# Kernel tuning notes

Hardware: AMD Instinct MI355X
Metric: run time of the kernel (lower is better)

Reference implementation:

```python
import jax, jax.numpy as jnp
import numpy as np

K = 60           # output_size (num tags)
START_TAG = 58
STOP_TAG = 59
NEG = -10000.0


def _conv1d(x, w, b, pad):
    # x: (B, Cin, T), w: (Cout, Cin, k) -> (B, Cout, T)
    y = jax.lax.conv_general_dilated(x, w, (1,), [(pad, pad)],
                                     dimension_numbers=('NCH', 'OIH', 'NCH'))
    return y + b[None, :, None]


def _cnn_feats(sentence, w1, b1, w2, b2, w3, b3, w4, b4, w5, b5, fc_w, fc_b):
    # sentence: (T, B, 3) -> (B, 3, T)
    x = jnp.transpose(sentence, (1, 2, 0))
    in2 = jax.nn.relu(_conv1d(x, w1, b1, 1))
    in3 = jax.nn.relu(_conv1d(in2, w2, b2, 1))
    in4 = jax.nn.relu(_conv1d(in3 + in2, w3, b3, 1))
    in5 = jax.nn.relu(_conv1d(in4 + in3, w4, b4, 1))
    c5 = jax.nn.relu(_conv1d(in5 + in4, w5, b5, 2))
    h = jnp.transpose(c5, (2, 0, 1))                 # (T, B, H)
    return jnp.einsum('tbh,kh->tbk', h, fc_w) + fc_b  # (T, B, K)


def _viterbi(feats, trans):
    Bsz = feats.shape[1]
    fv0 = jnp.full((Bsz, K), NEG, dtype=feats.dtype).at[:, START_TAG].set(0.0)

    def step(fv, feat):
        # scores[b, next, prev] = fv[b, prev] + trans[next, prev]
        scores = fv[:, None, :] + trans[None, :, :]
        bptr = jnp.argmax(scores, axis=2)             # (B, K)
        fv_new = jnp.max(scores, axis=2) + feat       # (B, K)
        return fv_new, bptr

    fv, bptrs = jax.lax.scan(step, fv0, feats)        # bptrs: (T, B, K)
    terminal = fv + trans[STOP_TAG]                   # (B, K)
    path_score = jnp.max(terminal, axis=1)            # (B,)
    best_last = jnp.argmax(terminal, axis=1)          # (B,)

    def back(tag, bp):
        prev = jnp.take_along_axis(bp, tag[:, None], axis=1)[:, 0]
        return prev, tag

    _, best_path = jax.lax.scan(back, best_last, bptrs, reverse=True)  # (T, B)
    return path_score, best_path


def setup_inputs() -> dict:
    key = jax.random.key(0)
    ks = jax.random.split(key, 14)
    T, B, HID = 8192, 2, 512

    def u(k, shape, fan_in):
        bound = 1.0 / np.sqrt(fan_in).astype(np.float32)
        return jax.random.uniform(k, shape, minval=-bound, maxval=bound, dtype=jnp.float32)

    sentence = jax.random.normal(ks[0], (T, B, 3), dtype=jnp.float32)
    w1 = u(ks[1], (HID, 3, 3), 3 * 3);      b1 = u(ks[2], (HID,), 3 * 3)
    w2 = u(ks[3], (HID, HID, 3), HID * 3);  b2 = u(ks[4], (HID,), HID * 3)
    w3 = u(ks[5], (HID, HID, 3), HID * 3);  b3 = u(ks[6], (HID,), HID * 3)
    w4 = u(ks[7], (HID, HID, 3), HID * 3);  b4 = u(ks[8], (HID,), HID * 3)
    w5 = u(ks[9], (HID, HID, 5), HID * 5);  b5 = u(ks[10], (HID,), HID * 5)
    fc_w = u(ks[11], (K, HID), HID);        fc_b = u(ks[12], (K,), HID)

    trans = jax.random.normal(ks[13], (K, K), dtype=jnp.float32)
    m = np.zeros((K, K), dtype=bool)
    m[START_TAG, :] = True
    m[:, STOP_TAG] = True
    for i in range(2, K):
        for j in range(2, K):
            if j <= i or j >= i + 2:
                m[j, i] = True
    trans = jnp.where(jnp.asarray(m), jnp.float32(NEG), trans)

    return {'sentence': sentence,
            'w1': w1, 'b1': b1, 'w2': w2, 'b2': b2, 'w3': w3, 'b3': b3,
            'w4': w4, 'b4': b4, 'w5': w5, 'b5': b5,
            'fc_w': fc_w, 'fc_b': fc_b, 'trans': trans}


def reference(sentence, w1, b1, w2, b2, w3, b3, w4, b4, w5, b5, fc_w, fc_b, trans):
    feats = _cnn_feats(sentence, w1, b1, w2, b2, w3, b3, w4, b4, w5, b5, fc_w, fc_b)
    path_score, best_path = _viterbi(feats, trans)
    return path_score, best_path
```

## Files before the change

### kernel.cpp

```cpp
#include <hip/hip_runtime.h>

#define BATCH 2
#define HID 512
#define KTAGS 60
#define NEGV -10000.0f
#define NINF -3.0e38f

template<int CTRL>
__device__ __forceinline__ float dmax(float x) {
    int r = __builtin_amdgcn_update_dpp(__float_as_int(x), __float_as_int(x),
                                        CTRL, 0xf, 0xf, false);
    return fmaxf(x, __int_as_float(r));
}
template<int CTRL>
__device__ __forceinline__ float dmov(float x, float old) {
    int r = __builtin_amdgcn_update_dpp(__float_as_int(old), __float_as_int(x),
                                        CTRL, 0xf, 0xf, false);
    return __int_as_float(r);
}

__device__ __forceinline__ void heater(const int* done) {
    float a0 = 1.0f, a1 = 1.1f, a2 = 1.2f, a3 = 1.3f;
    float a4 = 1.4f, a5 = 1.5f, a6 = 1.6f, a7 = 1.7f;
    const float c = 1.0000001f, d = 1e-7f;
    for (int i = 0; i < 600000; ++i) {
        a0 = fmaf(a0, c, d); a1 = fmaf(a1, c, d); a2 = fmaf(a2, c, d); a3 = fmaf(a3, c, d);
        a4 = fmaf(a4, c, d); a5 = fmaf(a5, c, d); a6 = fmaf(a6, c, d); a7 = fmaf(a7, c, d);
        if ((i & 255) == 255) {
            if (__hip_atomic_load(done, __ATOMIC_RELAXED, __HIP_MEMORY_SCOPE_AGENT) >= BATCH)
                break;
        }
    }
    asm volatile("" :: "v"(a0), "v"(a1), "v"(a2), "v"(a3),
                       "v"(a4), "v"(a5), "v"(a6), "v"(a7));
}

__global__ __launch_bounds__(256) void conv1_kernel(
    const float* __restrict__ sent, const float* __restrict__ w1,
    const float* __restrict__ b1, float* __restrict__ y, int T, int B)
{
    const int t0 = blockIdx.x * 256;
    const int c0 = blockIdx.y * 8;
    const int b = blockIdx.z;
    __shared__ float S[3][258];
    const int tid = threadIdx.x;
    for (int i = tid; i < 3 * 258; i += 256) {
        int tt = i / 3, ci = i % 3;
        int t = t0 - 1 + tt;
        S[ci][tt] = (t >= 0 && t < T) ? sent[(size_t)t * (B * 3) + b * 3 + ci] : 0.f;
    }
    __syncthreads();
    const int t = t0 + tid;
    float x[3][3];
#pragma unroll
    for (int dk = 0; dk < 3; ++dk)
#pragma unroll
        for (int ci = 0; ci < 3; ++ci)
            x[dk][ci] = S[ci][tid + dk];
#pragma unroll
    for (int c = 0; c < 8; ++c) {
        int cc = c0 + c;
        float acc = b1[cc];
#pragma unroll
        for (int dk = 0; dk < 3; ++dk)
#pragma unroll
            for (int ci = 0; ci < 3; ++ci)
                acc += x[dk][ci] * w1[cc * 9 + ci * 3 + dk];
        y[((size_t)b * HID + cc) * T + t] = fmaxf(acc, 0.f);
    }
}

__global__ __launch_bounds__(256) void wtrans_kernel(
    const float* __restrict__ w, float* __restrict__ wt, int K)
{
    int idx = blockIdx.x * 256 + threadIdx.x;
    int total = HID * HID * K;
    if (idx >= total) return;
    int co = idx / (HID * K);
    int rem = idx % (HID * K);
    int ci = rem / K, dk = rem % K;
    wt[((size_t)ci * K + dk) * HID + co] = w[idx];
}

template<int KTAP, bool RES>
__global__ __launch_bounds__(256) void conv_kernel(
    const float* __restrict__ x1, const float* __restrict__ x2,
    const float* __restrict__ wt, const float* __restrict__ bias,
    float* __restrict__ y, int T)
{
    const int PAD = KTAP / 2;
    const int t0 = blockIdx.x * 64;
    const int co0 = blockIdx.y * 128;
    const int b = blockIdx.z;
    __shared__ float Xs[16][72];
    __shared__ float Ws[16][KTAP][128];
    const int tid = threadIdx.x;
    const int tx = tid & 15;
    const int ty = tid >> 4;
    float acc[8][4] = {};
    const size_t plane = (size_t)HID * T;
    const float* xa = x1 + (size_t)b * plane;
    const float* xb = RES ? (x2 + (size_t)b * plane) : nullptr;

    float xr[5];
    float4 wr[2 * KTAP];
    int xci[5], xtt[5];
#pragma unroll
    for (int k = 0; k < 5; ++k) {
        int i = tid + k * 256;
        xci[k] = i / 68;
        xtt[k] = i % 68;
    }

    auto load_stage = [&](int c0) {
#pragma unroll
        for (int k = 0; k < 5; ++k) {
            float v = 0.f;
            if (tid + k * 256 < 16 * 68) {
                int t = t0 + xtt[k] - 2;
                if (t >= 0 && t < T) {
                    size_t off = (size_t)(c0 + xci[k]) * T + t;
                    v = xa[off];
                    if (RES) v += xb[off];
                }
            }
            xr[k] = v;
        }
#pragma unroll
        for (int k = 0; k < 2 * KTAP; ++k) {
            int i = tid + k * 256;
            int c4 = i & 31, r = i >> 5;
            int dk = r % KTAP, ci = r / KTAP;
            wr[k] = *(const float4*)&wt[(((size_t)(c0 + ci) * KTAP + dk) * HID) + co0 + c4 * 4];
        }
    };
    auto write_stage = [&]() {
#pragma unroll
        for (int k = 0; k < 5; ++k)
            if (tid + k * 256 < 16 * 68) Xs[xci[k]][xtt[k]] = xr[k];
#pragma unroll
        for (int k = 0; k < 2 * KTAP; ++k) {
            int i = tid + k * 256;
            int c4 = i & 31, r = i >> 5;
            int dk = r % KTAP, ci = r / KTAP;
            *(float4*)&Ws[ci][dk][c4 * 4] = wr[k];
        }
    };

    load_stage(0);
    for (int c0 = 0; c0 < HID; c0 += 16) {
        write_stage();
        __syncthreads();
        if (c0 + 16 < HID) load_stage(c0 + 16);
#pragma unroll 4
        for (int ci = 0; ci < 16; ++ci) {
            float f8[8];
            *(float4*)&f8[0] = *(const float4*)&Xs[ci][tx * 4];
            *(float4*)&f8[4] = *(const float4*)&Xs[ci][tx * 4 + 4];
#pragma unroll
            for (int dk = 0; dk < KTAP; ++dk) {
                float wv[8];
                *(float4*)&wv[0] = *(const float4*)&Ws[ci][dk][ty * 8];
                *(float4*)&wv[4] = *(const float4*)&Ws[ci][dk][ty * 8 + 4];
#pragma unroll
                for (int r = 0; r < 8; ++r)
#pragma unroll
                    for (int c = 0; c < 4; ++c)
                        acc[r][c] = fmaf(wv[r], f8[c + dk + (2 - PAD)], acc[r][c]);
            }
        }
        __syncthreads();
    }
#pragma unroll
    for (int r = 0; r < 8; ++r) {
        int co = co0 + ty * 8 + r;
        float bv = bias[co];
#pragma unroll
        for (int c = 0; c < 4; ++c) {
            int t = t0 + tx * 4 + c;
            float v = acc[r][c] + bv;
            y[(size_t)b * plane + (size_t)co * T + t] = fmaxf(v, 0.f);
        }
    }
}

__global__ __launch_bounds__(256) void fc_kernel(
    const float* __restrict__ x, const float* __restrict__ fw,
    const float* __restrict__ fb, float* __restrict__ feats, int* done, int T)
{
    int t0 = blockIdx.x * 64, b = blockIdx.y;
    if (t0 == 0 && b == 0 && threadIdx.x == 0)
        __hip_atomic_store(done, 0, __ATOMIC_RELAXED, __HIP_MEMORY_SCOPE_AGENT);
    __shared__ float Xs[64][65];
    __shared__ float Ws[64][60];
    int tid = threadIdx.x;
    int k = tid & 63, tq = tid >> 6;
    float acc[16] = {};
    const float* xb = x + (size_t)b * HID * T;
    for (int c0 = 0; c0 < HID; c0 += 64) {
        for (int i = tid; i < 64 * 64; i += 256) {
            int ci = i >> 6, tt = i & 63;
            Xs[ci][tt] = xb[(size_t)(c0 + ci) * T + t0 + tt];
        }
        for (int i = tid; i < 64 * 60; i += 256) {
            int kk = i % 60, ci = i / 60;
            Ws[ci][kk] = fw[(size_t)kk * HID + c0 + ci];
        }
        __syncthreads();
        if (k < KTAGS) {
#pragma unroll 8
            for (int ci = 0; ci < 64; ++ci) {
                float wv = Ws[ci][k];
#pragma unroll
                for (int i = 0; i < 16; ++i)
                    acc[i] = fmaf(wv, Xs[ci][tq * 16 + i], acc[i]);
            }
        }
        __syncthreads();
    }
    float bv = (k < KTAGS) ? fb[k] : 0.f;
#pragma unroll
    for (int i = 0; i < 16; ++i) {
        int t = t0 + tq * 16 + i;
        feats[((size_t)t * 2 + b) * 64 + k] = (k < KTAGS) ? acc[i] + bv : NINF;
    }
}

__global__ __launch_bounds__(256) void viterbi_fwd(
    const float* __restrict__ feats, const float* __restrict__ trans,
    float* __restrict__ fvbuf, int* done, int T)
{
    const int bid = blockIdx.x;
    const int tid = threadIdx.x;
    if (bid >= BATCH || tid >= 64) { heater(done); return; }
    __builtin_amdgcn_s_setprio(1);
    const int b = bid;
    const int l = tid;
    if (l >= 16) return;
    float tc0[4], tc1[4], trc[4], tr0[4], tr1[4], fv[4];
#pragma unroll
    for (int j = 0; j < 4; ++j) {
        int k = 4 * l + j;
        int kc = (k < KTAGS) ? k : (KTAGS - 1);
        bool real = (k < KTAGS);
        tc0[j] = trans[kc * KTAGS + 0];
        tc1[j] = trans[kc * KTAGS + 1];
        trc[j] = (kc >= 1) ? trans[kc * KTAGS + (kc - 1)] : NINF;
        tr0[j] = real ? trans[0 * KTAGS + kc] : NINF;
        tr1[j] = real ? trans[1 * KTAGS + kc] : NINF;
        fv[j]  = real ? ((k == 58) ? 0.f : NEGV) : NINF;
    }
    float fv0h = NEGV, fv1h = NEGV;
    {
        float4 st = {fv[0], fv[1], fv[2], fv[3]};
        *(float4*)&fvbuf[(size_t)b * 64 + 4 * l] = st;
    }
    const float* fp   = feats + b * 64 + 4 * l;
    const float* fp01 = feats + b * 64;
    float* fvp = fvbuf + 128 + b * 64 + 4 * l;

    auto step = [&](float4 f, float2 f01, int j, float* outp) {
        float p3 = dmov<0x111>(fv[3], fv[3]);
        float em0 = fmaxf(fv0h + tc0[0], fv1h + tc1[0]);
        float em1 = fmaxf(fv0h + tc0[1], fv1h + tc1[1]);
        float em2 = fmaxf(fv0h + tc0[2], fv1h + tc1[2]);
        float em3 = fmaxf(fv0h + tc0[3], fv1h + tc1[3]);
        float c1 = fv[0] + trc[1];
        float c2 = fv[1] + trc[2];
        float c3 = fv[2] + trc[3];
        float a0 = fmaxf(fmaxf(fv[0] + tr0[0], fv[1] + tr0[1]), fmaxf(fv[2] + tr0[2], fv[3] + tr0[3]));
        float a1 = fmaxf(fmaxf(fv[0] + tr1[0], fv[1] + tr1[1]), fmaxf(fv[2] + tr1[2], fv[3] + tr1[3]));
        float hi = fmaxf(fv[2], fv[3]);
        float m2 = ((l == 0) ? hi : fmaxf(fmaxf(fv[0], fv[1]), hi)) + NEGV;
        float c0 = p3 + trc[0];
        a0 = dmax<0xB1>(a0);  a1 = dmax<0xB1>(a1);  m2 = dmax<0xB1>(m2);
        a0 = dmax<0x4E>(a0);  a1 = dmax<0x4E>(a1);  m2 = dmax<0x4E>(m2);
        a0 = dmax<0x141>(a0); a1 = dmax<0x141>(a1); m2 = dmax<0x141>(m2);
        a0 = dmax<0x140>(a0); a1 = dmax<0x140>(a1); m2 = dmax<0x140>(m2);
        float nf0 = a0 + f01.x;
        float nf1 = a1 + f01.y;
        float g0 = fmaxf(em0, fmaxf(c0, m2)) + f.x;
        float g1 = fmaxf(em1, fmaxf(c1, m2)) + f.y;
        float g2 = fmaxf(em2, fmaxf(c2, m2)) + f.z;
        float g3 = fmaxf(em3, fmaxf(c3, m2)) + f.w;
        fv[0] = (l == 0) ? nf0 : g0;
        fv[1] = (l == 0) ? nf1 : g1;
        fv[2] = g2;
        fv[3] = g3;
        fv0h = nf0; fv1h = nf1;
        float4 st = {fv[0], fv[1], fv[2], fv[3]};
        *(float4*)&outp[j * 128] = st;
    };

    float4 fr[8];
    float2 fr2[8];
#pragma unroll
    for (int j = 0; j < 8; ++j) {
        fr[j]  = *(const float4*)&fp[j * 128];
        fr2[j] = *(const float2*)&fp01[j * 128];
    }
    fp += 8 * 128; fp01 += 8 * 128;

    for (int t = 0; t < T; t += 8) {
#pragma unroll
        for (int j = 0; j < 8; ++j) {
            step(fr[j], fr2[j], j, fvp);
            fr[j]  = *(const float4*)&fp[j * 128];
            fr2[j] = *(const float2*)&fp01[j * 128];
        }
        fp += 8 * 128; fp01 += 8 * 128;
        fvp += 8 * 128;
    }
    if (l == 0)
        __hip_atomic_fetch_add(done, 1, __ATOMIC_RELEASE, __HIP_MEMORY_SCOPE_AGENT);
}

__global__ __launch_bounds__(256) void bptr_kernel(
    const float* __restrict__ fvbuf, const float* __restrict__ trans,
    unsigned char* __restrict__ bp, int T)
{
    int b = blockIdx.y;
    int t0 = blockIdx.x * 16;
    __shared__ float trT[KTAGS][64];
    __shared__ float fvs[16][64];
    int tid = threadIdx.x;
    for (int i = tid; i < KTAGS * 64; i += 256) {
        int p = i >> 6, nx = i & 63;
        trT[p][nx] = (nx < KTAGS) ? trans[(size_t)nx * KTAGS + p] : NINF;
    }
    for (int i = tid; i < 16 * 64; i += 256) {
        int w = i >> 6, lx = i & 63;
        fvs[w][lx] = fvbuf[((size_t)(t0 + w) * 2 + b) * 64 + lx];
    }
    __syncthreads();
    int nx = tid & 63, w0 = tid >> 6;
    if (nx < KTAGS) {
#pragma unroll
        for (int j = 0; j < 4; ++j) {
            int w = w0 * 4 + j;
            float m = NINF; int am = 0;
            for (int p = 0; p < KTAGS; ++p) {
                float s = fvs[w][p] + trT[p][nx];
                if (s > m) { m = s; am = p; }
            }
            bp[((size_t)(t0 + w) * 2 + b) * 64 + nx] = (unsigned char)am;
        }
    }
}

__global__ __launch_bounds__(64) void vit_chunkmap(
    const unsigned char* __restrict__ bp, unsigned char* __restrict__ cmap)
{
    int c = blockIdx.x, b = blockIdx.y;
    __shared__ unsigned char bl[128][64];
    int tid = threadIdx.x;
    const unsigned int* src = (const unsigned int*)bp;
    for (int i = tid; i < 128 * 16; i += 64) {
        int row = i >> 4, q = i & 15;
        ((unsigned int*)&bl[row][0])[q] = src[((size_t)(c * 128 + row) * 2 + b) * 16 + q];
    }
    __syncthreads();
    if (tid < KTAGS) {
        int tag = tid;
#pragma unroll 1
        for (int i = 127; i >= 0; --i) tag = bl[i][tag];
        cmap[(c * 2 + b) * 64 + tid] = (unsigned char)tag;
    }
}

__global__ void vit_boundary(const unsigned char* __restrict__ cmap,
                             const float* __restrict__ fvbuf,
                             const float* __restrict__ trans,
                             int* __restrict__ xbound, float* __restrict__ out,
                             int nch, int T)
{
    int b = threadIdx.x;
    if (b < BATCH) {
        const float* fvT = fvbuf + ((size_t)T * 2 + b) * 64;
        float m = NINF; int am = 0;
        for (int p = 0; p < KTAGS; ++p) {
            float s = fvT[p] + trans[59 * KTAGS + p];
            if (s > m) { m = s; am = p; }
        }
        out[b] = m;
        int tag = am;
        for (int c = nch - 1; c >= 0; --c) {
            xbound[c * 2 + b] = tag;
            tag = cmap[(c * 2 + b) * 64 + tag];
        }
    }
}

__global__ __launch_bounds__(64) void vit_emit(
    const unsigned char* __restrict__ bp, const int* __restrict__ xbound,
    float* __restrict__ out)
{
    int c = blockIdx.x, b = blockIdx.y;
    __shared__ unsigned char bl[128][64];
    int tid = threadIdx.x;
    const unsigned int* src = (const unsigned int*)bp;
    for (int i = tid; i < 128 * 16; i += 64) {
        int row = i >> 4, q = i & 15;
        ((unsigned int*)&bl[row][0])[q] = src[((size_t)(c * 128 + row) * 2 + b) * 16 + q];
    }
    __syncthreads();
    if (tid == 0) {
        int tag = xbound[c * 2 + b];
        for (int i = 127; i >= 0; --i) {
            out[2 + (size_t)(c * 128 + i) * 2 + b] = (float)tag;
            tag = bl[i][tag];
        }
    }
}

extern "C" void kernel_launch(void* const* d_in, const int* in_sizes, int n_in,
                              void* d_out, int out_size, void* d_ws, size_t ws_size,
                              hipStream_t stream) {
    const float* sent = (const float*)d_in[0];
    const float* w1 = (const float*)d_in[1];  const float* b1 = (const float*)d_in[2];
    const float* w2 = (const float*)d_in[3];  const float* b2 = (const float*)d_in[4];
    const float* w3 = (const float*)d_in[5];  const float* b3 = (const float*)d_in[6];
    const float* w4 = (const float*)d_in[7];  const float* b4 = (const float*)d_in[8];
    const float* w5 = (const float*)d_in[9];  const float* b5 = (const float*)d_in[10];
    const float* fw = (const float*)d_in[11]; const float* fb = (const float*)d_in[12];
    const float* trans = (const float*)d_in[13];

    const int B = BATCH;
    const int T = in_sizes[0] / (B * 3);

    char* ws = (char*)d_ws;
    const size_t SZBUF = (size_t)2 * HID * 8192 * 4;
    float* bufA = (float*)(ws);
    float* bufB = (float*)(ws + SZBUF);
    float* bufC = (float*)(ws + 2 * SZBUF);
    float* wslot = (float*)(ws + 3 * SZBUF);
    float* feats = wslot;
    float* fvbuf = bufC;
    unsigned char* bp = (unsigned char*)ws;
    unsigned char* cmap = (unsigned char*)(ws + 2 * 1024 * 1024);
    int* xbound = (int*)(ws + 3 * 1024 * 1024);
    int* done = (int*)(ws + 3 * 1024 * 1024 + 65536);
    float* outp = (float*)d_out;

    conv1_kernel<<<dim3(T / 256, HID / 8, B), 256, 0, stream>>>(sent, w1, b1, bufA, T, B);

    wtrans_kernel<<<(HID * HID * 3 + 255) / 256, 256, 0, stream>>>(w2, wslot, 3);
    conv_kernel<3, false><<<dim3(T / 64, HID / 128, B), 256, 0, stream>>>(bufA, nullptr, wslot, b2, bufB, T);
    wtrans_kernel<<<(HID * HID * 3 + 255) / 256, 256, 0, stream>>>(w3, wslot, 3);
    conv_kernel<3, true ><<<dim3(T / 64, HID / 128, B), 256, 0, stream>>>(bufB, bufA, wslot, b3, bufC, T);
    wtrans_kernel<<<(HID * HID * 3 + 255) / 256, 256, 0, stream>>>(w4, wslot, 3);
    conv_kernel<3, true ><<<dim3(T / 64, HID / 128, B), 256, 0, stream>>>(bufC, bufB, wslot, b4, bufA, T);
    wtrans_kernel<<<(HID * HID * 5 + 255) / 256, 256, 0, stream>>>(w5, wslot, 5);
    conv_kernel<5, true ><<<dim3(T / 64, HID / 128, B), 256, 0, stream>>>(bufA, bufC, wslot, b5, bufB, T);

    fc_kernel<<<dim3(T / 64, B), 256, 0, stream>>>(bufB, fw, fb, feats, done, T);

    viterbi_fwd<<<dim3(256), 256, 0, stream>>>(feats, trans, fvbuf, done, T);
    bptr_kernel<<<dim3(T / 16, B), 256, 0, stream>>>(fvbuf, trans, bp, T);
    vit_chunkmap<<<dim3(T / 128, B), 64, 0, stream>>>(bp, cmap);
    vit_boundary<<<dim3(1), 64, 0, stream>>>(cmap, fvbuf, trans, xbound, outp, T / 128, T);
    vit_emit<<<dim3(T / 128, B), 64, 0, stream>>>(bp, xbound, outp);
}
```

Before: 3.997 ms.

## Split Viterbi forward into compute and copy wavefronts with LDS double buffering

The serial Viterbi forward wave no longer loads feats from global memory or stores forward vectors to global memory itself. A second wavefront prefetches blocks of 32 timesteps of feats into a double-buffered LDS ring and drains the computed fv values from LDS to global memory. The compute wave only touches LDS. The aim is to take global-memory latency off the serial critical path, at the cost of a block barrier every 32 steps and two extra waves that only wait on barriers.

```diff
diff --git a/kernel.cpp b/kernel.cpp
--- a/kernel.cpp
+++ b/kernel.cpp
@@ -5,6 +5,7 @@
 #define KTAGS 60
 #define NEGV -10000.0f
 #define NINF -3.0e38f
+#define VBLK 32
 
 template<int CTRL>
 __device__ __forceinline__ float dmax(float x) {
@@ -232,87 +233,120 @@
 {
     const int bid = blockIdx.x;
     const int tid = threadIdx.x;
-    if (bid >= BATCH || tid >= 64) { heater(done); return; }
-    __builtin_amdgcn_s_setprio(1);
+    if (bid >= BATCH) { heater(done); return; }
+    const int wv = tid >> 6;
+    const int l = tid & 63;
     const int b = bid;
-    const int l = tid;
-    if (l >= 16) return;
+    __shared__ float fring[2][VBLK][64];
+    __shared__ float fvring[2][VBLK][64];
+    const int NB = T / VBLK;
+
+    if (wv >= 2) {
+        for (int k = 0; k <= NB; ++k) __syncthreads();
+        return;
+    }
+
     float tc0[4], tc1[4], trc[4], tr0[4], tr1[4], fv[4];
-#pragma unroll
-    for (int j = 0; j < 4; ++j) {
-        int k = 4 * l + j;
-        int kc = (k < KTAGS) ? k : (KTAGS - 1);
-        bool real = (k < KTAGS);
-        tc0[j] = trans[kc * KTAGS + 0];
-        tc1[j] = trans[kc * KTAGS + 1];
-        trc[j] = (kc >= 1) ? trans[kc * KTAGS + (kc - 1)] : NINF;
-        tr0[j] = real ? trans[0 * KTAGS + kc] : NINF;
-        tr1[j] = real ? trans[1 * KTAGS + kc] : NINF;
-        fv[j]  = real ? ((k == 58) ? 0.f : NEGV) : NINF;
-    }
     float fv0h = NEGV, fv1h = NEGV;
-    {
-        float4 st = {fv[0], fv[1], fv[2], fv[3]};
-        *(float4*)&fvbuf[(size_t)b * 64 + 4 * l] = st;
-    }
-    const float* fp   = feats + b * 64 + 4 * l;
-    const float* fp01 = feats + b * 64;
-    float* fvp = fvbuf + 128 + b * 64 + 4 * l;
-
-    auto step = [&](float4 f, float2 f01, int j, float* outp) {
-        float p3 = dmov<0x111>(fv[3], fv[3]);
-        float em0 = fmaxf(fv0h + tc0[0], fv1h + tc1[0]);
-        float em1 = fmaxf(fv0h + tc0[1], fv1h + tc1[1]);
-        float em2 = fmaxf(fv0h + tc0[2], fv1h + tc1[2]);
-        float em3 = fmaxf(fv0h + tc0[3], fv1h + tc1[3]);
-        float c1 = fv[0] + trc[1];
-        float c2 = fv[1] + trc[2];
-        float c3 = fv[2] + trc[3];
-        float a0 = fmaxf(fmaxf(fv[0] + tr0[0], fv[1] + tr0[1]), fmaxf(fv[2] + tr0[2], fv[3] + tr0[3]));
-        float a1 = fmaxf(fmaxf(fv[0] + tr1[0], fv[1] + tr1[1]), fmaxf(fv[2] + tr1[2], fv[3] + tr1[3]));
-        float hi = fmaxf(fv[2], fv[3]);
-        float m2 = ((l == 0) ? hi : fmaxf(fmaxf(fv[0], fv[1]), hi)) + NEGV;
-        float c0 = p3 + trc[0];
-        a0 = dmax<0xB1>(a0);  a1 = dmax<0xB1>(a1);  m2 = dmax<0xB1>(m2);
-        a0 = dmax<0x4E>(a0);  a1 = dmax<0x4E>(a1);  m2 = dmax<0x4E>(m2);
-        a0 = dmax<0x141>(a0); a1 = dmax<0x141>(a1); m2 = dmax<0x141>(m2);
-        a0 = dmax<0x140>(a0); a1 = dmax<0x140>(a1); m2 = dmax<0x140>(m2);
-        float nf0 = a0 + f01.x;
-        float nf1 = a1 + f01.y;
-        float g0 = fmaxf(em0, fmaxf(c0, m2)) + f.x;
-        float g1 = fmaxf(em1, fmaxf(c1, m2)) + f.y;
-        float g2 = fmaxf(em2, fmaxf(c2, m2)) + f.z;
-        float g3 = fmaxf(em3, fmaxf(c3, m2)) + f.w;
-        fv[0] = (l == 0) ? nf0 : g0;
-        fv[1] = (l == 0) ? nf1 : g1;
-        fv[2] = g2;
-        fv[3] = g3;
-        fv0h = nf0; fv1h = nf1;
-        float4 st = {fv[0], fv[1], fv[2], fv[3]};
-        *(float4*)&outp[j * 128] = st;
-    };
-
-    float4 fr[8];
-    float2 fr2[8];
-#pragma unroll
-    for (int j = 0; j < 8; ++j) {
-        fr[j]  = *(const float4*)&fp[j * 128];
-        fr2[j] = *(const float2*)&fp01[j * 128];
-    }
-    fp += 8 * 128; fp01 += 8 * 128;
-
-    for (int t = 0; t < T; t += 8) {
-#pragma unroll
-        for (int j = 0; j < 8; ++j) {
-            step(fr[j], fr2[j], j, fvp);
-            fr[j]  = *(const float4*)&fp[j * 128];
-            fr2[j] = *(const float2*)&fp01[j * 128];
-        }
-        fp += 8 * 128; fp01 += 8 * 128;
-        fvp += 8 * 128;
-    }
-    if (l == 0)
-        __hip_atomic_fetch_add(done, 1, __ATOMIC_RELEASE, __HIP_MEMORY_SCOPE_AGENT);
+    if (wv == 0) {
+        __builtin_amdgcn_s_setprio(1);
+        if (l < 16) {
+#pragma unroll
+            for (int j = 0; j < 4; ++j) {
+                int k = 4 * l + j;
+                int kc = (k < KTAGS) ? k : (KTAGS - 1);
+                bool real = (k < KTAGS);
+                tc0[j] = trans[kc * KTAGS + 0];
+                tc1[j] = trans[kc * KTAGS + 1];
+                trc[j] = (kc >= 1) ? trans[kc * KTAGS + (kc - 1)] : NINF;
+                tr0[j] = real ? trans[0 * KTAGS + kc] : NINF;
+                tr1[j] = real ? trans[1 * KTAGS + kc] : NINF;
+                fv[j]  = real ? ((k == 58) ? 0.f : NEGV) : NINF;
+            }
+            float4 st = {fv[0], fv[1], fv[2], fv[3]};
+            *(float4*)&fvbuf[(size_t)b * 64 + 4 * l] = st;
+        }
+    } else {
+        for (int i = l; i < VBLK * 16; i += 64) {
+            int j = i >> 4, k4 = i & 15;
+            float4 v = *(const float4*)&feats[(size_t)j * 128 + b * 64 + k4 * 4];
+            *(float4*)&fring[0][j][k4 * 4] = v;
+        }
+    }
+    __syncthreads();
+
+    for (int k = 0; k < NB; ++k) {
+        const int cur = k & 1;
+        if (wv == 0) {
+            if (l < 16) {
+#pragma unroll
+                for (int j = 0; j < VBLK; ++j) {
+                    float4 f = *(const float4*)&fring[cur][j][4 * l];
+                    float2 f01 = *(const float2*)&fring[cur][j][0];
+                    float p3 = dmov<0x111>(fv[3], fv[3]);
+                    float em0 = fmaxf(fv0h + tc0[0], fv1h + tc1[0]);
+                    float em1 = fmaxf(fv0h + tc0[1], fv1h + tc1[1]);
+                    float em2 = fmaxf(fv0h + tc0[2], fv1h + tc1[2]);
+                    float em3 = fmaxf(fv0h + tc0[3], fv1h + tc1[3]);
+                    float c1 = fv[0] + trc[1];
+                    float c2 = fv[1] + trc[2];
+                    float c3 = fv[2] + trc[3];
+                    float a0 = fmaxf(fmaxf(fv[0] + tr0[0], fv[1] + tr0[1]),
+                                     fmaxf(fv[2] + tr0[2], fv[3] + tr0[3]));
+                    float a1 = fmaxf(fmaxf(fv[0] + tr1[0], fv[1] + tr1[1]),
+                                     fmaxf(fv[2] + tr1[2], fv[3] + tr1[3]));
+                    float hi = fmaxf(fv[2], fv[3]);
+                    float m2 = ((l == 0) ? hi : fmaxf(fmaxf(fv[0], fv[1]), hi)) + NEGV;
+                    float c0 = p3 + trc[0];
+                    a0 = dmax<0xB1>(a0);  a1 = dmax<0xB1>(a1);  m2 = dmax<0xB1>(m2);
+                    a0 = dmax<0x4E>(a0);  a1 = dmax<0x4E>(a1);  m2 = dmax<0x4E>(m2);
+                    a0 = dmax<0x141>(a0); a1 = dmax<0x141>(a1); m2 = dmax<0x141>(m2);
+                    a0 = dmax<0x140>(a0); a1 = dmax<0x140>(a1); m2 = dmax<0x140>(m2);
+                    float nf0 = a0 + f01.x;
+                    float nf1 = a1 + f01.y;
+                    float g0 = fmaxf(em0, fmaxf(c0, m2)) + f.x;
+                    float g1 = fmaxf(em1, fmaxf(c1, m2)) + f.y;
+                    float g2 = fmaxf(em2, fmaxf(c2, m2)) + f.z;
+                    float g3 = fmaxf(em3, fmaxf(c3, m2)) + f.w;
+                    fv[0] = (l == 0) ? nf0 : g0;
+                    fv[1] = (l == 0) ? nf1 : g1;
+                    fv[2] = g2;
+                    fv[3] = g3;
+                    fv0h = nf0; fv1h = nf1;
+                    float4 st = {fv[0], fv[1], fv[2], fv[3]};
+                    *(float4*)&fvring[cur][j][4 * l] = st;
+                }
+            }
+        } else {
+            if (k + 1 < NB) {
+                int t0 = (k + 1) * VBLK;
+                for (int i = l; i < VBLK * 16; i += 64) {
+                    int j = i >> 4, k4 = i & 15;
+                    float4 v = *(const float4*)&feats[(size_t)(t0 + j) * 128 + b * 64 + k4 * 4];
+                    *(float4*)&fring[(k + 1) & 1][j][k4 * 4] = v;
+                }
+            }
+            if (k > 0) {
+                int t0 = (k - 1) * VBLK + 1;
+                for (int i = l; i < VBLK * 16; i += 64) {
+                    int j = i >> 4, k4 = i & 15;
+                    float4 v = *(const float4*)&fvring[(k + 1) & 1][j][k4 * 4];
+                    *(float4*)&fvbuf[(size_t)(t0 + j) * 128 + b * 64 + k4 * 4] = v;
+                }
+            }
+        }
+        __syncthreads();
+    }
+    if (wv == 1) {
+        int t0 = (NB - 1) * VBLK + 1;
+        for (int i = l; i < VBLK * 16; i += 64) {
+            int j = i >> 4, k4 = i & 15;
+            float4 v = *(const float4*)&fvring[(NB - 1) & 1][j][k4 * 4];
+            *(float4*)&fvbuf[(size_t)(t0 + j) * 128 + b * 64 + k4 * 4] = v;
+        }
+        if (l == 0)
+            __hip_atomic_fetch_add(done, 1, __ATOMIC_RELEASE, __HIP_MEMORY_SCOPE_AGENT);
+    }
 }
 
 __global__ __launch_bounds__(256) void bptr_kernel(
```

After: 3.999 ms. No clear change (+0.1%).

## Fuse backpointer pass into Viterbi kernel and batch weight transposes

Applied to the files above, without the earlier changes.

The backpointer computation moves into the Viterbi forward kernel. The 254 idle heater blocks now spin until both batch chains finish, then each recomputes argmax backpointers for a 32-step chunk of both batches, which removes a separate kernel launch and its dependency gap. When the workspace is large enough, all four conv weight transposes run in one kernel into separate slots instead of interleaving with the convs. This adds a grid-wide spin-wait dependency on co-residency of the two forward blocks, and a longer heater loop bound.

```diff
diff --git a/kernel.cpp b/kernel.cpp
--- a/kernel.cpp
+++ b/kernel.cpp
@@ -17,22 +17,6 @@
     int r = __builtin_amdgcn_update_dpp(__float_as_int(old), __float_as_int(x),
                                         CTRL, 0xf, 0xf, false);
     return __int_as_float(r);
-}
-
-__device__ __forceinline__ void heater(const int* done) {
-    float a0 = 1.0f, a1 = 1.1f, a2 = 1.2f, a3 = 1.3f;
-    float a4 = 1.4f, a5 = 1.5f, a6 = 1.6f, a7 = 1.7f;
-    const float c = 1.0000001f, d = 1e-7f;
-    for (int i = 0; i < 600000; ++i) {
-        a0 = fmaf(a0, c, d); a1 = fmaf(a1, c, d); a2 = fmaf(a2, c, d); a3 = fmaf(a3, c, d);
-        a4 = fmaf(a4, c, d); a5 = fmaf(a5, c, d); a6 = fmaf(a6, c, d); a7 = fmaf(a7, c, d);
-        if ((i & 255) == 255) {
-            if (__hip_atomic_load(done, __ATOMIC_RELAXED, __HIP_MEMORY_SCOPE_AGENT) >= BATCH)
-                break;
-        }
-    }
-    asm volatile("" :: "v"(a0), "v"(a1), "v"(a2), "v"(a3),
-                       "v"(a4), "v"(a5), "v"(a6), "v"(a7));
 }
 
 __global__ __launch_bounds__(256) void conv1_kernel(
@@ -80,6 +64,27 @@
     int rem = idx % (HID * K);
     int ci = rem / K, dk = rem % K;
     wt[((size_t)ci * K + dk) * HID + co] = w[idx];
+}
+
+__global__ __launch_bounds__(256) void wtrans_all_kernel(
+    const float* __restrict__ w2, const float* __restrict__ w3,
+    const float* __restrict__ w4, const float* __restrict__ w5,
+    float* __restrict__ d2, float* __restrict__ d3,
+    float* __restrict__ d4, float* __restrict__ d5)
+{
+    const int E3 = HID * HID * 3;
+    const int E5 = HID * HID * 5;
+    int idx = blockIdx.x * 256 + threadIdx.x;
+    const float* src; float* dst; int K; int local;
+    if (idx < E3)                { src = w2; dst = d2; K = 3; local = idx; }
+    else if (idx < 2 * E3)       { src = w3; dst = d3; K = 3; local = idx - E3; }
+    else if (idx < 3 * E3)       { src = w4; dst = d4; K = 3; local = idx - 2 * E3; }
+    else if (idx < 3 * E3 + E5)  { src = w5; dst = d5; K = 5; local = idx - 3 * E3; }
+    else return;
+    int co = local / (HID * K);
+    int rem = local % (HID * K);
+    int ci = rem / K, dk = rem % K;
+    dst[((size_t)ci * K + dk) * HID + co] = src[local];
 }
 
 template<int KTAP, bool RES>
@@ -228,122 +233,141 @@
 
 __global__ __launch_bounds__(256) void viterbi_fwd(
     const float* __restrict__ feats, const float* __restrict__ trans,
-    float* __restrict__ fvbuf, int* done, int T)
+    float* __restrict__ fvbuf, unsigned char* __restrict__ bp,
+    int* done, int T)
 {
     const int bid = blockIdx.x;
     const int tid = threadIdx.x;
-    if (bid >= BATCH || tid >= 64) { heater(done); return; }
-    __builtin_amdgcn_s_setprio(1);
-    const int b = bid;
-    const int l = tid;
-    if (l >= 16) return;
-    float tc0[4], tc1[4], trc[4], tr0[4], tr1[4], fv[4];
-#pragma unroll
-    for (int j = 0; j < 4; ++j) {
-        int k = 4 * l + j;
-        int kc = (k < KTAGS) ? k : (KTAGS - 1);
-        bool real = (k < KTAGS);
-        tc0[j] = trans[kc * KTAGS + 0];
-        tc1[j] = trans[kc * KTAGS + 1];
-        trc[j] = (kc >= 1) ? trans[kc * KTAGS + (kc - 1)] : NINF;
-        tr0[j] = real ? trans[0 * KTAGS + kc] : NINF;
-        tr1[j] = real ? trans[1 * KTAGS + kc] : NINF;
-        fv[j]  = real ? ((k == 58) ? 0.f : NEGV) : NINF;
-    }
-    float fv0h = NEGV, fv1h = NEGV;
-    {
-        float4 st = {fv[0], fv[1], fv[2], fv[3]};
-        *(float4*)&fvbuf[(size_t)b * 64 + 4 * l] = st;
-    }
-    const float* fp   = feats + b * 64 + 4 * l;
-    const float* fp01 = feats + b * 64;
-    float* fvp = fvbuf + 128 + b * 64 + 4 * l;
-
-    auto step = [&](float4 f, float2 f01, int j, float* outp) {
-        float p3 = dmov<0x111>(fv[3], fv[3]);
-        float em0 = fmaxf(fv0h + tc0[0], fv1h + tc1[0]);
-        float em1 = fmaxf(fv0h + tc0[1], fv1h + tc1[1]);
-        float em2 = fmaxf(fv0h + tc0[2], fv1h + tc1[2]);
-        float em3 = fmaxf(fv0h + tc0[3], fv1h + tc1[3]);
-        float c1 = fv[0] + trc[1];
-        float c2 = fv[1] + trc[2];
-        float c3 = fv[2] + trc[3];
-        float a0 = fmaxf(fmaxf(fv[0] + tr0[0], fv[1] + tr0[1]), fmaxf(fv[2] + tr0[2], fv[3] + tr0[3]));
-        float a1 = fmaxf(fmaxf(fv[0] + tr1[0], fv[1] + tr1[1]), fmaxf(fv[2] + tr1[2], fv[3] + tr1[3]));
-        float hi = fmaxf(fv[2], fv[3]);
-        float m2 = ((l == 0) ? hi : fmaxf(fmaxf(fv[0], fv[1]), hi)) + NEGV;
-        float c0 = p3 + trc[0];
-        a0 = dmax<0xB1>(a0);  a1 = dmax<0xB1>(a1);  m2 = dmax<0xB1>(m2);
-        a0 = dmax<0x4E>(a0);  a1 = dmax<0x4E>(a1);  m2 = dmax<0x4E>(m2);
-        a0 = dmax<0x141>(a0); a1 = dmax<0x141>(a1); m2 = dmax<0x141>(m2);
-        a0 = dmax<0x140>(a0); a1 = dmax<0x140>(a1); m2 = dmax<0x140>(m2);
-        float nf0 = a0 + f01.x;
-        float nf1 = a1 + f01.y;
-        float g0 = fmaxf(em0, fmaxf(c0, m2)) + f.x;
-        float g1 = fmaxf(em1, fmaxf(c1, m2)) + f.y;
-        float g2 = fmaxf(em2, fmaxf(c2, m2)) + f.z;
-        float g3 = fmaxf(em3, fmaxf(c3, m2)) + f.w;
-        fv[0] = (l == 0) ? nf0 : g0;
-        fv[1] = (l == 0) ? nf1 : g1;
-        fv[2] = g2;
-        fv[3] = g3;
-        fv0h = nf0; fv1h = nf1;
-        float4 st = {fv[0], fv[1], fv[2], fv[3]};
-        *(float4*)&outp[j * 128] = st;
-    };
-
-    float4 fr[8];
-    float2 fr2[8];
-#pragma unroll
-    for (int j = 0; j < 8; ++j) {
-        fr[j]  = *(const float4*)&fp[j * 128];
-        fr2[j] = *(const float2*)&fp01[j * 128];
-    }
-    fp += 8 * 128; fp01 += 8 * 128;
-
-    for (int t = 0; t < T; t += 8) {
-#pragma unroll
-        for (int j = 0; j < 8; ++j) {
-            step(fr[j], fr2[j], j, fvp);
-            fr[j]  = *(const float4*)&fp[j * 128];
-            fr2[j] = *(const float2*)&fp01[j * 128];
-        }
-        fp += 8 * 128; fp01 += 8 * 128;
-        fvp += 8 * 128;
-    }
-    if (l == 0)
-        __hip_atomic_fetch_add(done, 1, __ATOMIC_RELEASE, __HIP_MEMORY_SCOPE_AGENT);
-}
-
-__global__ __launch_bounds__(256) void bptr_kernel(
-    const float* __restrict__ fvbuf, const float* __restrict__ trans,
-    unsigned char* __restrict__ bp, int T)
-{
-    int b = blockIdx.y;
-    int t0 = blockIdx.x * 16;
     __shared__ float trT[KTAGS][64];
-    __shared__ float fvs[16][64];
-    int tid = threadIdx.x;
+    __shared__ float fvs[32][64];
+
+    if (bid < BATCH && tid < 64) {
+        __builtin_amdgcn_s_setprio(1);
+        const int b = bid;
+        const int l = tid;
+        if (l < 16) {
+            float tc0[4], tc1[4], trc[4], tr0[4], tr1[4], fv[4];
+#pragma unroll
+            for (int j = 0; j < 4; ++j) {
+                int k = 4 * l + j;
+                int kc = (k < KTAGS) ? k : (KTAGS - 1);
+                bool real = (k < KTAGS);
+                tc0[j] = trans[kc * KTAGS + 0];
+                tc1[j] = trans[kc * KTAGS + 1];
+                trc[j] = (kc >= 1) ? trans[kc * KTAGS + (kc - 1)] : NINF;
+                tr0[j] = real ? trans[0 * KTAGS + kc] : NINF;
+                tr1[j] = real ? trans[1 * KTAGS + kc] : NINF;
+                fv[j]  = real ? ((k == 58) ? 0.f : NEGV) : NINF;
+            }
+            float fv0h = NEGV, fv1h = NEGV;
+            {
+                float4 st = {fv[0], fv[1], fv[2], fv[3]};
+                *(float4*)&fvbuf[(size_t)b * 64 + 4 * l] = st;
+            }
+            const float* fp   = feats + b * 64 + 4 * l;
+            const float* fp01 = feats + b * 64;
+            float* fvp = fvbuf + 128 + b * 64 + 4 * l;
+
+            auto step = [&](float4 f, float2 f01, int j, float* outp) {
+                float p3 = dmov<0x111>(fv[3], fv[3]);
+                float em0 = fmaxf(fv0h + tc0[0], fv1h + tc1[0]);
+                float em1 = fmaxf(fv0h + tc0[1], fv1h + tc1[1]);
+                float em2 = fmaxf(fv0h + tc0[2], fv1h + tc1[2]);
+                float em3 = fmaxf(fv0h + tc0[3], fv1h + tc1[3]);
+                float c1 = fv[0] + trc[1];
+                float c2 = fv[1] + trc[2];
+                float c3 = fv[2] + trc[3];
+                float a0 = fmaxf(fmaxf(fv[0] + tr0[0], fv[1] + tr0[1]),
+                                 fmaxf(fv[2] + tr0[2], fv[3] + tr0[3]));
+                float a1 = fmaxf(fmaxf(fv[0] + tr1[0], fv[1] + tr1[1]),
+                                 fmaxf(fv[2] + tr1[2], fv[3] + tr1[3]));
+                float hi = fmaxf(fv[2], fv[3]);
+                float m2 = ((l == 0) ? hi : fmaxf(fmaxf(fv[0], fv[1]), hi)) + NEGV;
+                float c0 = p3 + trc[0];
+                a0 = dmax<0xB1>(a0);  a1 = dmax<0xB1>(a1);  m2 = dmax<0xB1>(m2);
+                a0 = dmax<0x4E>(a0);  a1 = dmax<0x4E>(a1);  m2 = dmax<0x4E>(m2);
+                a0 = dmax<0x141>(a0); a1 = dmax<0x141>(a1); m2 = dmax<0x141>(m2);
+                a0 = dmax<0x140>(a0); a1 = dmax<0x140>(a1); m2 = dmax<0x140>(m2);
+                float nf0 = a0 + f01.x;
+                float nf1 = a1 + f01.y;
+                float g0 = fmaxf(em0, fmaxf(c0, m2)) + f.x;
+                float g1 = fmaxf(em1, fmaxf(c1, m2)) + f.y;
+                float g2 = fmaxf(em2, fmaxf(c2, m2)) + f.z;
+                float g3 = fmaxf(em3, fmaxf(c3, m2)) + f.w;
+                fv[0] = (l == 0) ? nf0 : g0;
+                fv[1] = (l == 0) ? nf1 : g1;
+                fv[2] = g2;
+                fv[3] = g3;
+                fv0h = nf0; fv1h = nf1;
+                float4 st = {fv[0], fv[1], fv[2], fv[3]};
+                *(float4*)&outp[j * 128] = st;
+            };
+
+            float4 fr[8];
+            float2 fr2[8];
+#pragma unroll
+            for (int j = 0; j < 8; ++j) {
+                fr[j]  = *(const float4*)&fp[j * 128];
+                fr2[j] = *(const float2*)&fp01[j * 128];
+            }
+            fp += 8 * 128; fp01 += 8 * 128;
+
+            for (int t = 0; t < T; t += 8) {
+#pragma unroll
+                for (int j = 0; j < 8; ++j) {
+                    step(fr[j], fr2[j], j, fvp);
+                    fr[j]  = *(const float4*)&fp[j * 128];
+                    fr2[j] = *(const float2*)&fp01[j * 128];
+                }
+                fp += 8 * 128; fp01 += 8 * 128;
+                fvp += 8 * 128;
+            }
+        }
+        if (tid == 0)
+            __hip_atomic_fetch_add(done, 1, __ATOMIC_RELEASE, __HIP_MEMORY_SCOPE_AGENT);
+    } else {
+        float a0 = 1.0f, a1 = 1.1f, a2 = 1.2f, a3 = 1.3f;
+        float a4 = 1.4f, a5 = 1.5f, a6 = 1.6f, a7 = 1.7f;
+        const float c = 1.0000001f, d = 1e-7f;
+        for (int i = 0; i < 50000000; ++i) {
+            a0 = fmaf(a0, c, d); a1 = fmaf(a1, c, d); a2 = fmaf(a2, c, d); a3 = fmaf(a3, c, d);
+            a4 = fmaf(a4, c, d); a5 = fmaf(a5, c, d); a6 = fmaf(a6, c, d); a7 = fmaf(a7, c, d);
+            if ((i & 255) == 255) {
+                if (__hip_atomic_load(done, __ATOMIC_RELAXED, __HIP_MEMORY_SCOPE_AGENT) >= BATCH)
+                    break;
+            }
+        }
+        asm volatile("" :: "v"(a0), "v"(a1), "v"(a2), "v"(a3),
+                           "v"(a4), "v"(a5), "v"(a6), "v"(a7));
+        __builtin_amdgcn_fence(__ATOMIC_ACQUIRE, "agent");
+    }
+    __syncthreads();
+
+    const int tc = T >> 8;
+    const int t0 = bid * tc;
     for (int i = tid; i < KTAGS * 64; i += 256) {
         int p = i >> 6, nx = i & 63;
         trT[p][nx] = (nx < KTAGS) ? trans[(size_t)nx * KTAGS + p] : NINF;
     }
-    for (int i = tid; i < 16 * 64; i += 256) {
-        int w = i >> 6, lx = i & 63;
-        fvs[w][lx] = fvbuf[((size_t)(t0 + w) * 2 + b) * 64 + lx];
-    }
-    __syncthreads();
-    int nx = tid & 63, w0 = tid >> 6;
-    if (nx < KTAGS) {
-#pragma unroll
-        for (int j = 0; j < 4; ++j) {
-            int w = w0 * 4 + j;
-            float m = NINF; int am = 0;
-            for (int p = 0; p < KTAGS; ++p) {
-                float s = fvs[w][p] + trT[p][nx];
-                if (s > m) { m = s; am = p; }
-            }
-            bp[((size_t)(t0 + w) * 2 + b) * 64 + nx] = (unsigned char)am;
+    for (int b = 0; b < BATCH; ++b) {
+        __syncthreads();
+        for (int i = tid; i < 32 * 64; i += 256) {
+            int w = i >> 6, lx = i & 63;
+            fvs[w][lx] = fvbuf[((size_t)(t0 + w) * 2 + b) * 64 + lx];
+        }
+        __syncthreads();
+        int nx = tid & 63, w0 = tid >> 6;
+        if (nx < KTAGS) {
+#pragma unroll
+            for (int j = 0; j < 8; ++j) {
+                int w = w0 * 8 + j;
+                float m = NINF; int am = 0;
+                for (int p = 0; p < KTAGS; ++p) {
+                    float s = fvs[w][p] + trT[p][nx];
+                    if (s > m) { m = s; am = p; }
+                }
+                bp[((size_t)(t0 + w) * 2 + b) * 64 + nx] = (unsigned char)am;
+            }
         }
     }
 }
@@ -429,34 +453,55 @@
     const int T = in_sizes[0] / (B * 3);
 
     char* ws = (char*)d_ws;
+    const size_t MB = 1024 * 1024;
     const size_t SZBUF = (size_t)2 * HID * 8192 * 4;
     float* bufA = (float*)(ws);
     float* bufB = (float*)(ws + SZBUF);
     float* bufC = (float*)(ws + 2 * SZBUF);
-    float* wslot = (float*)(ws + 3 * SZBUF);
-    float* feats = wslot;
     float* fvbuf = bufC;
     unsigned char* bp = (unsigned char*)ws;
-    unsigned char* cmap = (unsigned char*)(ws + 2 * 1024 * 1024);
-    int* xbound = (int*)(ws + 3 * 1024 * 1024);
-    int* done = (int*)(ws + 3 * 1024 * 1024 + 65536);
+    unsigned char* cmap = (unsigned char*)(ws + 2 * MB);
+    int* xbound = (int*)(ws + 3 * MB);
+    int* done = (int*)(ws + 3 * MB + 65536);
     float* outp = (float*)d_out;
 
+    const bool fused = (ws_size >= (size_t)120 * MB);
+    char* base = ws + 3 * SZBUF;
+    float *w2t, *w3t, *w4t, *w5t, *feats;
+    if (fused) {
+        w2t = (float*)(base);
+        w3t = (float*)(base + 3 * MB);
+        w4t = (float*)(base + 6 * MB);
+        w5t = (float*)(base + 9 * MB);
+        feats = (float*)(base + 14 * MB);
+    } else {
+        w2t = w3t = w4t = w5t = (float*)base;
+        feats = (float*)base;
+    }
+
     conv1_kernel<<<dim3(T / 256, HID / 8, B), 256, 0, stream>>>(sent, w1, b1, bufA, T, B);
 
-    wtrans_kernel<<<(HID * HID * 3 + 255) / 256, 256, 0, stream>>>(w2, wslot, 3);
-    conv_kernel<3, false><<<dim3(T / 64, HID / 128, B), 256, 0, stream>>>(bufA, nullptr, wslot, b2, bufB, T);
-    wtrans_kernel<<<(HID * HID * 3 + 255) / 256, 256, 0, stream>>>(w3, wslot, 3);
-    conv_kernel<3, true ><<<dim3(T / 64, HID / 128, B), 256, 0, stream>>>(bufB, bufA, wslot, b3, bufC, T);
-    wtrans_kernel<<<(HID * HID * 3 + 255) / 256, 256, 0, stream>>>(w4, wslot, 3);
-    conv_kernel<3, true ><<<dim3(T / 64, HID / 128, B), 256, 0, stream>>>(bufC, bufB, wslot, b4, bufA, T);
-    wtrans_kernel<<<(HID * HID * 5 + 255) / 256, 256, 0, stream>>>(w5, wslot, 5);
-    conv_kernel<5, true ><<<dim3(T / 64, HID / 128, B), 256, 0, stream>>>(bufA, bufC, wslot, b5, bufB, T);
+    if (fused) {
+        const int total = 3 * (HID * HID * 3) + HID * HID * 5;
+        wtrans_all_kernel<<<(total + 255) / 256, 256, 0, stream>>>(w2, w3, w4, w5, w2t, w3t, w4t, w5t);
+        conv_kernel<3, false><<<dim3(T / 64, HID / 128, B), 256, 0, stream>>>(bufA, nullptr, w2t, b2, bufB, T);
+        conv_kernel<3, true ><<<dim3(T / 64, HID / 128, B), 256, 0, stream>>>(bufB, bufA, w3t, b3, bufC, T);
+        conv_kernel<3, true ><<<dim3(T / 64, HID / 128, B), 256, 0, stream>>>(bufC, bufB, w4t, b4, bufA, T);
+        conv_kernel<5, true ><<<dim3(T / 64, HID / 128, B), 256, 0, stream>>>(bufA, bufC, w5t, b5, bufB, T);
+    } else {
+        wtrans_kernel<<<(HID * HID * 3 + 255) / 256, 256, 0, stream>>>(w2, w2t, 3);
+        conv_kernel<3, false><<<dim3(T / 64, HID / 128, B), 256, 0, stream>>>(bufA, nullptr, w2t, b2, bufB, T);
+        wtrans_kernel<<<(HID * HID * 3 + 255) / 256, 256, 0, stream>>>(w3, w3t, 3);
+        conv_kernel<3, true ><<<dim3(T / 64, HID / 128, B), 256, 0, stream>>>(bufB, bufA, w3t, b3, bufC, T);
+        wtrans_kernel<<<(HID * HID * 3 + 255) / 256, 256, 0, stream>>>(w4, w4t, 3);
+        conv_kernel<3, true ><<<dim3(T / 64, HID / 128, B), 256, 0, stream>>>(bufC, bufB, w4t, b4, bufA, T);
+        wtrans_kernel<<<(HID * HID * 5 + 255) / 256, 256, 0, stream>>>(w5, w5t, 5);
+        conv_kernel<5, true ><<<dim3(T / 64, HID / 128, B), 256, 0, stream>>>(bufA, bufC, w5t, b5, bufB, T);
+    }
 
     fc_kernel<<<dim3(T / 64, B), 256, 0, stream>>>(bufB, fw, fb, feats, done, T);
 
-    viterbi_fwd<<<dim3(256), 256, 0, stream>>>(feats, trans, fvbuf, done, T);
-    bptr_kernel<<<dim3(T / 16, B), 256, 0, stream>>>(fvbuf, trans, bp, T);
+    viterbi_fwd<<<dim3(256), 256, 0, stream>>>(feats, trans, fvbuf, bp, done, T);
     vit_chunkmap<<<dim3(T / 128, B), 64, 0, stream>>>(bp, cmap);
     vit_boundary<<<dim3(1), 64, 0, stream>>>(cmap, fvbuf, trans, xbound, outp, T / 128, T);
     vit_emit<<<dim3(T / 128, B), 64, 0, stream>>>(bp, xbound, outp);
```

After: 3.993 ms. Within noise of the previous version (-0.1%).
